# Kernel optimization log

Hardware: AMD Instinct MI355X
Metric: run time of the kernel (lower is better)

## Reference

```python
import jax, jax.numpy as jnp
import numpy as np

B, D, L = 4, 512, 4096
N1, N2 = 1167, 8921


def setup_inputs() -> dict:
    key = jax.random.key(0)
    k1, k2, k3, k4 = jax.random.split(key, 4)
    H = jax.random.normal(k1, (B, D, L), dtype=jnp.float32)
    Q1_w = jax.random.normal(k2, (N1, D), dtype=jnp.float32) * (1.0 / np.sqrt(D))
    Q2_w = jax.random.normal(k3, (N2, D), dtype=jnp.float32) * (1.0 / np.sqrt(D))
    Q12_w = jax.random.normal(k4, (N2, N1), dtype=jnp.float32) * (1.0 / np.sqrt(N1))
    return {"H": H, "Q1_w": Q1_w, "Q2_w": Q2_w, "Q12_w": Q12_w}


def reference(H, Q1_w, Q2_w, Q12_w):
    # H: [b, d, l]; Q1_w: [n1, d]; Q2_w: [n2, d]; Q12_w: [n2, n1]
    # Level-1 label attention
    E1 = jnp.einsum('nd,bdl->bnl', Q1_w, H)          # [b, n1, l]
    A1 = jax.nn.softmax(E1, axis=2)
    C1 = jnp.einsum('bnl,bdl->bnd', A1, H)           # [b, n1, d]
    # Project level-1 context to level-2 label space
    C1 = jnp.einsum('mn,bnd->bmd', Q12_w, C1)        # [b, n2, d]
    # Level-2 queries modulated by level-1 context (elementwise)
    Q2 = Q2_w[None, :, :] * C1                       # [b, n2, d]
    E2 = jnp.einsum('bmd,bdl->bml', Q2, H)           # [b, n2, l]
    A2 = jax.nn.softmax(E2, axis=2)
    C2 = jnp.einsum('bml,bdl->bmd', A2, H)           # [b, n2, d]
    return (C2, A2)
```

## Files before the change

### kernel.cpp

```cpp
#include <hip/hip_runtime.h>
#include <hip/hip_bf16.h>

typedef __bf16 bf16_t;
typedef __bf16 bf16x8 __attribute__((ext_vector_type(8)));
typedef __bf16 bf16x4 __attribute__((ext_vector_type(4)));
typedef float  f32x4  __attribute__((ext_vector_type(4)));

#define BM 128
#define BN 128
#define BK 64

__global__ __launch_bounds__(256) void cast_transpose_H(
    const float* __restrict__ H, bf16_t* __restrict__ Hb,
    bf16_t* __restrict__ HTb, int D, int L) {
  __shared__ bf16_t tile[32][33];
  int b = blockIdx.z;
  int l0 = blockIdx.x * 32, d0 = blockIdx.y * 32;
  const float* Hp = H + (size_t)b * D * L;
  bf16_t* Hbp = Hb + (size_t)b * D * L;
  bf16_t* HTp = HTb + (size_t)b * L * D;
  int tx = threadIdx.x, ty = threadIdx.y;
#pragma unroll
  for (int r = 0; r < 4; r++) {
    int d = d0 + ty + r * 8;
    float v = Hp[(size_t)d * L + l0 + tx];
    bf16_t bv = (bf16_t)v;
    tile[ty + r * 8][tx] = bv;
    Hbp[(size_t)d * L + l0 + tx] = bv;
  }
  __syncthreads();
#pragma unroll
  for (int r = 0; r < 4; r++) {
    int l = l0 + ty + r * 8;
    HTp[(size_t)l * D + d0 + tx] = tile[tx][ty + r * 8];
  }
}

__global__ void cast_w(const float* __restrict__ in, bf16_t* __restrict__ out, int n) {
  int i = blockIdx.x * 256 + threadIdx.x;
  if (i < n) out[i] = (bf16_t)in[i];
}

__global__ void cast_w_pad(const float* __restrict__ in, bf16_t* __restrict__ out,
                           int cols, int ldo) {
  int c = blockIdx.x * 256 + threadIdx.x;
  int r = blockIdx.y;
  if (c < ldo) {
    float v = (c < cols) ? in[(size_t)r * cols + c] : 0.0f;
    out[(size_t)r * ldo + c] = (bf16_t)v;
  }
}

__global__ void zero_pad(bf16_t* __restrict__ p, int n1, int ld, int rows) {
  int i = blockIdx.x * 256 + threadIdx.x;
  int padw = ld - n1;
  int r = i / padw, c = i - r * padw;
  if (r < rows) p[(size_t)r * ld + n1 + c] = (bf16_t)0.0f;
}

__device__ inline bf16x8 cvt8(float4 a, float4 b) {
  bf16x8 o;
  o[0] = (bf16_t)a.x; o[1] = (bf16_t)a.y; o[2] = (bf16_t)a.z; o[3] = (bf16_t)a.w;
  o[4] = (bf16_t)b.x; o[5] = (bf16_t)b.y; o[6] = (bf16_t)b.z; o[7] = (bf16_t)b.w;
  return o;
}

__device__ inline void gload_lds16(const bf16_t* g, bf16_t* l) {
  __builtin_amdgcn_global_load_lds(
      (const __attribute__((address_space(1))) void*)g,
      (__attribute__((address_space(3))) void*)l, 16, 0, 0);
}

template <typename AT, int EPI>
__global__ __launch_bounds__(256) void gemm_bt(
    const AT* __restrict__ A, long sAb, const bf16_t* __restrict__ BT, long sBb,
    void* __restrict__ Cv, long sCb, const float* __restrict__ W,
    int M, int N, int K, int lda, int ldb, int ldc) {
  constexpr bool AF32 = (sizeof(AT) == 4);
  __shared__ __align__(16) bf16_t As[BM][BK];
  __shared__ __align__(16) bf16_t Bs[BN][BK];
  int b = blockIdx.z;
  A += (size_t)b * sAb;
  BT += (size_t)b * sBb;

  int nx = gridDim.x, ny = gridDim.y;
  int nwg = nx * ny;
  int bid = blockIdx.x + nx * blockIdx.y;
  int qq = nwg >> 3, rr = nwg & 7;
  int xcd = bid & 7, lin = bid >> 3;
  int swz = (xcd < rr ? xcd * (qq + 1) : rr * (qq + 1) + (xcd - rr) * qq) + lin;
  int m0 = (swz / ny) * BM;
  int n0 = (swz % ny) * BN;

  int t = threadIdx.x;
  int lane = t & 63, wid = t >> 6;
  int l15 = lane & 15, q = lane >> 4;
  int wm = (wid >> 1) * 64, wn = (wid & 1) * 64;

  int r0 = t >> 3;
  int sl = t & 7;
  int gsl = sl ^ (r0 & 7);
  bf16_t* lA = &As[0][0] + (size_t)wid * 512;
  bf16_t* lB = &Bs[0][0] + (size_t)wid * 512;

  f32x4 acc[4][4];
#pragma unroll
  for (int i = 0; i < 4; i++)
#pragma unroll
    for (int j = 0; j < 4; j++)
#pragma unroll
      for (int e = 0; e < 4; e++) acc[i][j][e] = 0.0f;

  for (int kb = 0; kb < K; kb += BK) {
    float4 va[4][2];
    if constexpr (AF32) {
#pragma unroll
      for (int i = 0; i < 4; i++) {
        int gm = m0 + i * 32 + r0;
        if (gm < M) {
          const float4* p = (const float4*)(A + (size_t)gm * lda + kb + gsl * 8);
          va[i][0] = p[0];
          va[i][1] = p[1];
        } else {
          va[i][0] = make_float4(0.f, 0.f, 0.f, 0.f);
          va[i][1] = make_float4(0.f, 0.f, 0.f, 0.f);
        }
      }
    }
    __syncthreads();
#pragma unroll
    for (int i = 0; i < 4; i++)
      gload_lds16(BT + (size_t)(n0 + i * 32 + r0) * ldb + kb + gsl * 8,
                  lB + i * 2048);
    if constexpr (AF32) {
#pragma unroll
      for (int i = 0; i < 4; i++)
        *(bf16x8*)(&As[0][0] + (size_t)(i * 256 + t) * 8) = cvt8(va[i][0], va[i][1]);
    } else {
#pragma unroll
      for (int i = 0; i < 4; i++)
        gload_lds16(A + (size_t)(m0 + i * 32 + r0) * lda + kb + gsl * 8,
                    lA + i * 2048);
    }
    __syncthreads();

#pragma unroll
    for (int ks = 0; ks < 2; ks++) {
      bf16x8 af[4], bfr[4];
#pragma unroll
      for (int i = 0; i < 4; i++) {
        int row = wm + i * 16 + l15;
        int off = (ks * 64 + q * 16) ^ ((l15 & 7) << 4);
        af[i] = *(const bf16x8*)((const char*)&As[row][0] + off);
      }
#pragma unroll
      for (int j = 0; j < 4; j++) {
        int row = wn + j * 16 + l15;
        int off = (ks * 64 + q * 16) ^ ((l15 & 7) << 4);
        bfr[j] = *(const bf16x8*)((const char*)&Bs[row][0] + off);
      }
#pragma unroll
      for (int i = 0; i < 4; i++)
#pragma unroll
        for (int j = 0; j < 4; j++)
          acc[i][j] = __builtin_amdgcn_mfma_f32_16x16x32_bf16(af[i], bfr[j],
                                                              acc[i][j], 0, 0, 0);
    }
  }

#pragma unroll
  for (int i = 0; i < 4; i++) {
    int rbase = m0 + wm + i * 16 + q * 4;
#pragma unroll
    for (int j = 0; j < 4; j++) {
      int c = n0 + wn + j * 16 + l15;
#pragma unroll
      for (int r4 = 0; r4 < 4; r4++) {
        int r = rbase + r4;
        if (r < M) {
          float val = acc[i][j][r4];
          if (EPI == 0) {
            float* Cp = (float*)Cv + (size_t)b * sCb;
            Cp[(size_t)r * ldc + c] = val;
          } else if (EPI == 1) {
            bf16_t* Cp = (bf16_t*)Cv + (size_t)b * sCb;
            Cp[(size_t)c * ldc + r] = (bf16_t)val;
          } else {
            float w = W[(size_t)r * N + c];
            bf16_t* Cp = (bf16_t*)Cv + (size_t)b * sCb;
            Cp[(size_t)r * ldc + c] = (bf16_t)(val * w);
          }
        }
      }
    }
  }
}

template <int MODE>
__global__ __launch_bounds__(256) void softmax_rows(
    const float* __restrict__ in, void* __restrict__ out,
    bf16_t* __restrict__ out2, int L) {
  int row = blockIdx.x;
  const float* ip = in + (size_t)row * L;
  int t = threadIdx.x;
  int lane = t & 63, wid = t >> 6;
  float4 v[4];
  float m = -3.4e38f;
#pragma unroll
  for (int c = 0; c < 4; c++) {
    v[c] = ((const float4*)ip)[c * 256 + t];
    m = fmaxf(m, fmaxf(fmaxf(v[c].x, v[c].y), fmaxf(v[c].z, v[c].w)));
  }
#pragma unroll
  for (int off = 1; off < 64; off <<= 1) m = fmaxf(m, __shfl_xor(m, off));
  __shared__ float redm[4];
  __shared__ float reds[4];
  if (lane == 0) redm[wid] = m;
  __syncthreads();
  m = fmaxf(fmaxf(redm[0], redm[1]), fmaxf(redm[2], redm[3]));
  float s = 0.0f;
#pragma unroll
  for (int c = 0; c < 4; c++) {
    v[c].x = __expf(v[c].x - m);
    v[c].y = __expf(v[c].y - m);
    v[c].z = __expf(v[c].z - m);
    v[c].w = __expf(v[c].w - m);
    s += (v[c].x + v[c].y) + (v[c].z + v[c].w);
  }
#pragma unroll
  for (int off = 1; off < 64; off <<= 1) s += __shfl_xor(s, off);
  if (lane == 0) reds[wid] = s;
  __syncthreads();
  s = (reds[0] + reds[1]) + (reds[2] + reds[3]);
  float inv = 1.0f / s;
  if (MODE == 1) {
    bf16_t* op = (bf16_t*)out + (size_t)row * L;
#pragma unroll
    for (int c = 0; c < 4; c++) {
      bf16x4 o;
      o[0] = (bf16_t)(v[c].x * inv);
      o[1] = (bf16_t)(v[c].y * inv);
      o[2] = (bf16_t)(v[c].z * inv);
      o[3] = (bf16_t)(v[c].w * inv);
      *(bf16x4*)(op + ((size_t)c * 256 + t) * 4) = o;
    }
  } else {
    float* op = (float*)out + (size_t)row * L;
#pragma unroll
    for (int c = 0; c < 4; c++) {
      float fx = v[c].x * inv, fy = v[c].y * inv, fz = v[c].z * inv, fw = v[c].w * inv;
      ((float4*)op)[c * 256 + t] = make_float4(fx, fy, fz, fw);
      if (MODE == 2) {
        bf16x4 o;
        o[0] = (bf16_t)fx; o[1] = (bf16_t)fy; o[2] = (bf16_t)fz; o[3] = (bf16_t)fw;
        *(bf16x4*)(out2 + (size_t)row * L + ((size_t)c * 256 + t) * 4) = o;
      }
    }
  }
}

extern "C" void kernel_launch(void* const* d_in, const int* in_sizes, int n_in,
                              void* d_out, int out_size, void* d_ws, size_t ws_size,
                              hipStream_t stream) {
  const int B = 4, D = 512, L = 4096, N1 = 1167, N2 = 8921;
  const int N1K = 1216;
  const int M1P = 1280;
  const int M2P = 8960;
  const float* H = (const float*)d_in[0];
  const float* Q1w = (const float*)d_in[1];
  const float* Q2w = (const float*)d_in[2];
  const float* Q12w = (const float*)d_in[3];
  float* C2 = (float*)d_out;
  float* A2 = C2 + (size_t)B * N2 * D;

  char* ws = (char*)d_ws;
  size_t off = 0;
  auto alloc = [&](size_t bytes) -> void* {
    void* p = ws + off;
    off = (off + bytes + 255) & ~(size_t)255;
    return p;
  };
  bf16_t* Hb   = (bf16_t*)alloc((size_t)B * D * L * 2);
  bf16_t* HTb  = (bf16_t*)alloc((size_t)B * L * D * 2);
  bf16_t* Q1b  = (bf16_t*)alloc((size_t)M1P * D * 2);
  bf16_t* Q12b = (bf16_t*)alloc((size_t)M2P * N1K * 2);
  float*  E1   = (float*)alloc((size_t)B * N1 * L * 4);
  bf16_t* A1b  = (bf16_t*)alloc(((size_t)B * N1 + 128) * L * 2);
  bf16_t* C1Tb = (bf16_t*)alloc((size_t)B * D * N1K * 2);
  bf16_t* Q2b  = (bf16_t*)alloc(((size_t)B * N2 + 64) * D * 2);
  size_t a2b_bytes = ((size_t)B * N2 + 128) * (size_t)L * 2;
  bool useA2b = (ws_size > 0) && (off + a2b_bytes <= ws_size);
  bf16_t* A2b = (bf16_t*)alloc(a2b_bytes);

  cast_transpose_H<<<dim3(L / 32, D / 32, B), dim3(32, 8), 0, stream>>>(H, Hb, HTb, D, L);
  cast_w<<<(N1 * D + 255) / 256, 256, 0, stream>>>(Q1w, Q1b, N1 * D);
  cast_w_pad<<<dim3((N1K + 255) / 256, N2), 256, 0, stream>>>(Q12w, Q12b, N1, N1K);
  zero_pad<<<(B * D * (N1K - N1) + 255) / 256, 256, 0, stream>>>(C1Tb, N1, N1K, B * D);
  gemm_bt<bf16_t, 0><<<dim3(M1P / BM, L / BN, B), 256, 0, stream>>>(
      Q1b, 0, HTb, (long)L * D, E1, (long)N1 * L, nullptr, N1, L, D, D, D, L);
  softmax_rows<1><<<B * N1, 256, 0, stream>>>(E1, A1b, nullptr, L);
  gemm_bt<bf16_t, 1><<<dim3(M1P / BM, D / BN, B), 256, 0, stream>>>(
      A1b, (long)N1 * L, Hb, (long)D * L, C1Tb, (long)D * N1K, nullptr, N1, D, L, L, L, N1K);
  gemm_bt<bf16_t, 2><<<dim3(M2P / BM, D / BN, B), 256, 0, stream>>>(
      Q12b, 0, C1Tb, (long)D * N1K, Q2b, (long)N2 * D, Q2w, N2, D, N1K, N1K, N1K, D);
  gemm_bt<bf16_t, 0><<<dim3(M2P / BM, L / BN, B), 256, 0, stream>>>(
      Q2b, (long)N2 * D, HTb, (long)L * D, A2, (long)N2 * L, nullptr, N2, L, D, D, D, L);
  if (useA2b) {
    softmax_rows<2><<<B * N2, 256, 0, stream>>>(A2, A2, A2b, L);
    gemm_bt<bf16_t, 0><<<dim3(M2P / BM, D / BN, B), 256, 0, stream>>>(
        A2b, (long)N2 * L, Hb, (long)D * L, C2, (long)N2 * D, nullptr, N2, D, L, L, L, D);
  } else {
    softmax_rows<0><<<B * N2, 256, 0, stream>>>(A2, A2, nullptr, L);
    gemm_bt<float, 0><<<dim3(M2P / BM, D / BN, B), 256, 0, stream>>>(
        A2, (long)N2 * L, Hb, (long)D * L, C2, (long)N2 * D, nullptr, N2, D, L, L, L, D);
  }
}
```

Measured before the change: 1.755 ms.

## Add 256x256 tile bf16 GEMM with double-buffered async LDS staging

Adds a new 512-thread GEMM kernel with 256x256 output tiles. It double-buffers operands in LDS using direct global-to-LDS loads with an XOR swizzle, and interleaves staging with four MFMA quadrants per k-step. Four of the five GEMMs now use it, which raises data reuse per tile and overlaps memory traffic with compute. In exchange the grid has fewer, larger workgroups, which can hurt occupancy and tail balance, and the epilogue relies on M1P/M2P being padded to multiples of 256.

New measurement: 1.713 ms. -2.4%, faster.

```diff
diff --git a/kernel.cpp b/kernel.cpp
--- a/kernel.cpp
+++ b/kernel.cpp
@@ -69,6 +69,148 @@
   __builtin_amdgcn_global_load_lds(
       (const __attribute__((address_space(1))) void*)g,
       (__attribute__((address_space(3))) void*)l, 16, 0, 0);
+}
+
+__device__ inline void stage_half(const bf16_t* __restrict__ src, int ld,
+                                  bf16_t* lds_half, int t, int wid) {
+  int r = t >> 3;
+  int gsl = (t & 7) ^ (r & 7);
+  const bf16_t* g = src + (size_t)r * ld + gsl * 8;
+  gload_lds16(g, lds_half + wid * 512);
+  gload_lds16(g + (size_t)64 * ld, lds_half + 4096 + wid * 512);
+}
+
+template <int EPI>
+__global__ __launch_bounds__(512) void gemm256_bt(
+    const bf16_t* __restrict__ A, long sAb, const bf16_t* __restrict__ BT, long sBb,
+    void* __restrict__ Cv, long sCb, const float* __restrict__ W,
+    int M, int N, int K, int lda, int ldb, int ldc) {
+  __shared__ __align__(16) bf16_t As[2][256][64];
+  __shared__ __align__(16) bf16_t Bs[2][256][64];
+  int b = blockIdx.z;
+  A += (size_t)b * sAb;
+  BT += (size_t)b * sBb;
+
+  int nx = gridDim.x, ny = gridDim.y;
+  int nwg = nx * ny;
+  int bid = blockIdx.x + nx * blockIdx.y;
+  int qq = nwg >> 3, rr = nwg & 7;
+  int xcd = bid & 7, lin = bid >> 3;
+  int swz = (xcd < rr ? xcd * (qq + 1) : rr * (qq + 1) + (xcd - rr) * qq) + lin;
+  int m0 = (swz / ny) * 256;
+  int n0 = (swz % ny) * 256;
+
+  int t = threadIdx.x;
+  int lane = t & 63, wid = t >> 6;
+  int l15 = lane & 15, q = lane >> 4;
+  int wm = (wid >> 2) * 128;
+  int wn = (wid & 3) * 64;
+  int NT = K >> 6;
+
+  f32x4 acc[8][4];
+#pragma unroll
+  for (int i = 0; i < 8; i++)
+#pragma unroll
+    for (int j = 0; j < 4; j++)
+#pragma unroll
+      for (int e = 0; e < 4; e++) acc[i][j][e] = 0.0f;
+
+  stage_half(BT + (size_t)(n0 + 0) * ldb, ldb, &Bs[0][0][0], t, wid);
+  stage_half(BT + (size_t)(n0 + 128) * ldb, ldb, &Bs[0][128][0], t, wid);
+  stage_half(A + (size_t)(m0 + 0) * lda, lda, &As[0][0][0], t, wid);
+  stage_half(A + (size_t)(m0 + 128) * lda, lda, &As[0][128][0], t, wid);
+  stage_half(BT + (size_t)(n0 + 0) * ldb + 64, ldb, &Bs[1][0][0], t, wid);
+  stage_half(BT + (size_t)(n0 + 128) * ldb + 64, ldb, &Bs[1][128][0], t, wid);
+  asm volatile("s_waitcnt vmcnt(4)" ::: "memory");
+  __builtin_amdgcn_s_barrier();
+
+  bf16x8 af[4][2];
+  bf16x8 bF[2][2][2];
+
+  for (int kt = 0; kt < NT; ++kt) {
+    int buf = kt & 1;
+    const bf16_t* An = A + (size_t)m0 * lda + (size_t)(kt + 1) * 64;
+    const bf16_t* Bn2 = BT + (size_t)n0 * ldb + (size_t)(kt + 2) * 64;
+
+    auto readA = [&](int mh) {
+#pragma unroll
+      for (int i = 0; i < 4; i++) {
+        const char* rowp = (const char*)&As[buf][wm + mh * 64 + i * 16 + l15][0];
+#pragma unroll
+        for (int ks = 0; ks < 2; ks++)
+          af[i][ks] = *(const bf16x8*)(rowp + ((((ks * 4 + q) ^ (l15 & 7))) << 4));
+      }
+    };
+    auto readB = [&](int ch) {
+#pragma unroll
+      for (int j = 0; j < 2; j++) {
+        const char* rowp = (const char*)&Bs[buf][wn + ch * 32 + j * 16 + l15][0];
+#pragma unroll
+        for (int ks = 0; ks < 2; ks++)
+          bF[ch][j][ks] = *(const bf16x8*)(rowp + ((((ks * 4 + q) ^ (l15 & 7))) << 4));
+      }
+    };
+    auto mmaq = [&](int mh, int ch) {
+      __builtin_amdgcn_s_setprio(1);
+#pragma unroll
+      for (int i = 0; i < 4; i++)
+#pragma unroll
+        for (int j = 0; j < 2; j++)
+#pragma unroll
+          for (int ks = 0; ks < 2; ks++)
+            acc[mh * 4 + i][ch * 2 + j] = __builtin_amdgcn_mfma_f32_16x16x32_bf16(
+                af[i][ks], bF[ch][j][ks], acc[mh * 4 + i][ch * 2 + j], 0, 0, 0);
+      __builtin_amdgcn_s_setprio(0);
+    };
+
+    readA(0);
+    readB(0);
+    if (kt + 1 < NT) stage_half(An, lda, &As[buf ^ 1][0][0], t, wid);
+    __builtin_amdgcn_s_barrier();
+    mmaq(0, 0);
+    __builtin_amdgcn_s_barrier();
+    readB(1);
+    if (kt + 1 < NT) stage_half(An + (size_t)128 * lda, lda, &As[buf ^ 1][128][0], t, wid);
+    __builtin_amdgcn_s_barrier();
+    mmaq(0, 1);
+    __builtin_amdgcn_s_barrier();
+    readA(1);
+    if (kt + 2 < NT) stage_half(Bn2, ldb, &Bs[buf][0][0], t, wid);
+    __builtin_amdgcn_s_barrier();
+    mmaq(1, 0);
+    __builtin_amdgcn_s_barrier();
+    if (kt + 2 < NT) {
+      stage_half(Bn2 + (size_t)128 * ldb, ldb, &Bs[buf][128][0], t, wid);
+      asm volatile("s_waitcnt vmcnt(4)" ::: "memory");
+    } else if (kt + 1 < NT) {
+      asm volatile("s_waitcnt vmcnt(0)" ::: "memory");
+    }
+    __builtin_amdgcn_s_barrier();
+    mmaq(1, 1);
+    __builtin_amdgcn_s_barrier();
+  }
+
+#pragma unroll
+  for (int ig = 0; ig < 8; ig++) {
+    int rbase = m0 + wm + ig * 16 + q * 4;
+#pragma unroll
+    for (int jg = 0; jg < 4; jg++) {
+      int c = n0 + wn + jg * 16 + l15;
+#pragma unroll
+      for (int r4 = 0; r4 < 4; r4++) {
+        int r = rbase + r4;
+        if (r < M) {
+          float val = acc[ig][jg][r4];
+          if (EPI == 0) {
+            ((float*)Cv + (size_t)b * sCb)[(size_t)r * ldc + c] = val;
+          } else {
+            float w = W[(size_t)r * N + c];
+            ((bf16_t*)Cv + (size_t)b * sCb)[(size_t)r * ldc + c] = (bf16_t)(val * w);
+          }
+        }
+      }
+    }
+  }
 }
 
 template <typename AT, int EPI>
@@ -296,18 +438,18 @@
   cast_w<<<(N1 * D + 255) / 256, 256, 0, stream>>>(Q1w, Q1b, N1 * D);
   cast_w_pad<<<dim3((N1K + 255) / 256, N2), 256, 0, stream>>>(Q12w, Q12b, N1, N1K);
   zero_pad<<<(B * D * (N1K - N1) + 255) / 256, 256, 0, stream>>>(C1Tb, N1, N1K, B * D);
-  gemm_bt<bf16_t, 0><<<dim3(M1P / BM, L / BN, B), 256, 0, stream>>>(
+  gemm256_bt<0><<<dim3(M1P / 256, L / 256, B), 512, 0, stream>>>(
       Q1b, 0, HTb, (long)L * D, E1, (long)N1 * L, nullptr, N1, L, D, D, D, L);
   softmax_rows<1><<<B * N1, 256, 0, stream>>>(E1, A1b, nullptr, L);
   gemm_bt<bf16_t, 1><<<dim3(M1P / BM, D / BN, B), 256, 0, stream>>>(
       A1b, (long)N1 * L, Hb, (long)D * L, C1Tb, (long)D * N1K, nullptr, N1, D, L, L, L, N1K);
-  gemm_bt<bf16_t, 2><<<dim3(M2P / BM, D / BN, B), 256, 0, stream>>>(
+  gemm256_bt<2><<<dim3(M2P / 256, D / 256, B), 512, 0, stream>>>(
       Q12b, 0, C1Tb, (long)D * N1K, Q2b, (long)N2 * D, Q2w, N2, D, N1K, N1K, N1K, D);
-  gemm_bt<bf16_t, 0><<<dim3(M2P / BM, L / BN, B), 256, 0, stream>>>(
+  gemm256_bt<0><<<dim3(M2P / 256, L / 256, B), 512, 0, stream>>>(
       Q2b, (long)N2 * D, HTb, (long)L * D, A2, (long)N2 * L, nullptr, N2, L, D, D, D, L);
   if (useA2b) {
     softmax_rows<2><<<B * N2, 256, 0, stream>>>(A2, A2, A2b, L);
-    gemm_bt<bf16_t, 0><<<dim3(M2P / BM, D / BN, B), 256, 0, stream>>>(
+    gemm256_bt<0><<<dim3(M2P / 256, D / 256, B), 512, 0, stream>>>(
         A2b, (long)N2 * L, Hb, (long)D * L, C2, (long)N2 * D, nullptr, N2, D, L, L, L, D);
   } else {
     softmax_rows<0><<<B * N2, 256, 0, stream>>>(A2, A2, nullptr, L);
```
